# Kernel optimization log

Hardware: AMD Instinct MI355X
Metric: run time of the kernel (lower is better)

The kernel has to match this reference:

```python
import jax, jax.numpy as jnp
import numpy as np

NHEADS = 8
LN_EPS = 1e-5

def _layer_norm(x, g, b):
    mu = jnp.mean(x, axis=-1, keepdims=True)
    var = jnp.mean((x - mu) ** 2, axis=-1, keepdims=True)
    return (x - mu) * jax.lax.rsqrt(var + LN_EPS) * g + b

def setup_inputs() -> dict:
    key = jax.random.key(0)
    ks = jax.random.split(key, 12)
    B, L, D = 8, 1024, 512
    F = 2 * D  # ffn_dim = 2*dim
    std = 0.01  # init_weights: Linear weights ~ N(0, 0.01), biases zero
    inp = {
        'query': jax.random.normal(ks[0], (B, L, D), dtype=jnp.float32),
        'q_mask': jnp.ones((B, L), dtype=jnp.int32),
        'wq': jax.random.normal(ks[1], (D, D), dtype=jnp.float32) * std,
        'bq': jnp.zeros((D,), dtype=jnp.float32),
        'wk': jax.random.normal(ks[2], (D, D), dtype=jnp.float32) * std,
        'bk': jnp.zeros((D,), dtype=jnp.float32),
        'wv': jax.random.normal(ks[3], (D, D), dtype=jnp.float32) * std,
        'bv': jnp.zeros((D,), dtype=jnp.float32),
        'wo': jax.random.normal(ks[4], (D, D), dtype=jnp.float32) * std,
        'bo': jnp.zeros((D,), dtype=jnp.float32),
        'ln1_g': jnp.ones((D,), dtype=jnp.float32),
        'ln1_b': jnp.zeros((D,), dtype=jnp.float32),
        'w1': jax.random.normal(ks[5], (D, F), dtype=jnp.float32) * std,
        'b1': jnp.zeros((F,), dtype=jnp.float32),
        'w2': jax.random.normal(ks[6], (F, D), dtype=jnp.float32) * std,
        'b2': jnp.zeros((D,), dtype=jnp.float32),
        'ln2_g': jnp.ones((D,), dtype=jnp.float32),
        'ln2_b': jnp.zeros((D,), dtype=jnp.float32),
    }
    return inp

def reference(query, q_mask, wq, bq, wk, bk, wv, bv, wo, bo, ln1_g, ln1_b, w1, b1, w2, b2, ln2_g, ln2_b):
    B, L, D = query.shape
    H = NHEADS
    dh = D // H
    residual = query
    # projections (dropout in eval mode -> identity)
    q = query @ wq + bq
    k = query @ wk + bk
    v = query @ wv + bv
    # faithful to torch .view(batch*nheads, -1, dim_head) (no head transpose)
    q = q.reshape(B * H, L, dh)
    k = k.reshape(B * H, L, dh)
    v = v.reshape(B * H, L, dh)
    # faithful to torch mask.repeat(nheads, 1) -> tile along batch dim
    mf = q_mask.astype(jnp.float32)
    qm = jnp.tile(mf, (H, 1))  # [B*H, L]
    km = qm
    mask = qm[:, :, None] * km[:, None, :]  # [B*H, L, L] outer product
    scores = jnp.einsum('bqd,bkd->bqk', q, k) / np.sqrt(dh).astype(np.float32)
    A = jnp.where(mask == 0, 0.0, jnp.exp(scores))  # masked_fill(-inf).exp()
    A_sum = jnp.maximum(jnp.sum(A, axis=-1, keepdims=True), 1.0)
    attn = A / A_sum
    context = jnp.einsum('bqk,bkd->bqd', attn, v).reshape(B, L, H * dh)
    out = context @ wo + bo
    out = _layer_norm(residual + out, ln1_g, ln1_b)
    # positional-wise FFN: Linear -> ReLU -> Linear, residual + LayerNorm
    ffn = jax.nn.relu(out @ w1 + b1) @ w2 + b2
    out2 = _layer_norm(out + ffn, ln2_g, ln2_b)
    return (out2, q_mask, query, query, q_mask)
```

## Files before the change

kernel.cpp:

```cpp
#include <hip/hip_runtime.h>
#include <hip/hip_bf16.h>

typedef __hip_bfloat16 bf16;
typedef __attribute__((ext_vector_type(4))) float f32x4;
typedef __attribute__((ext_vector_type(8))) short s16x8;

#define MFMA(a, b, c) __builtin_amdgcn_mfma_f32_16x16x32_bf16((a), (b), (c), 0, 0, 0)

__device__ __forceinline__ void g2l16(const bf16* g, bf16* l) {
  __builtin_amdgcn_global_load_lds((const __attribute__((address_space(1))) void*)g,
                                   (__attribute__((address_space(3))) void*)l,
                                   16, 0, 0);
}
__device__ __forceinline__ bf16 cvt_bf(float f) { return __float2bfloat16(f); }
__device__ __forceinline__ float bf2f(bf16 h) { return __bfloat162float(h); }

__global__ __launch_bounds__(256)
void wcvt_all_k(const float* __restrict__ wq, const float* __restrict__ wk,
                const float* __restrict__ wv, const float* __restrict__ wo,
                const float* __restrict__ w1, const float* __restrict__ w2,
                bf16* __restrict__ wqkvT, bf16* __restrict__ woT,
                bf16* __restrict__ w1T, bf16* __restrict__ w2T)
{
  __shared__ float tl[32][33];
  const int bid = blockIdx.x;
  const float* W; bf16* Wt; int K, N, tile;
  if (bid < 768)        { int s = bid >> 8; W = s==0?wq:(s==1?wk:wv);
                          Wt = wqkvT + s*262144; K = 512; N = 512; tile = bid & 255; }
  else if (bid < 1024)  { W = wo; Wt = woT; K = 512;  N = 512;  tile = bid - 768; }
  else if (bid < 1536)  { W = w1; Wt = w1T; K = 512;  N = 1024; tile = bid - 1024; }
  else                  { W = w2; Wt = w2T; K = 1024; N = 512;  tile = bid - 1536; }
  const int nx = N >> 5;
  const int n0 = (tile % nx) * 32, k0 = (tile / nx) * 32;
  const int tx = threadIdx.x & 31, ty = threadIdx.x >> 5;
#pragma unroll
  for (int i = 0; i < 32; i += 8)
    tl[ty + i][tx] = W[(size_t)(k0 + ty + i) * N + n0 + tx];
  __syncthreads();
#pragma unroll
  for (int i = 0; i < 32; i += 8)
    Wt[(size_t)(n0 + ty + i) * K + k0 + tx] = cvt_bf(tl[tx][ty + i]);
}

__global__ __launch_bounds__(256)
void cvt_k(const float* __restrict__ in, bf16* __restrict__ o)
{
  const int i = (blockIdx.x * 256 + threadIdx.x) * 8;
  float4 a = *(const float4*)(in + i);
  float4 b = *(const float4*)(in + i + 4);
  union { bf16 h[8]; s16x8 v; } u;
  u.h[0] = cvt_bf(a.x); u.h[1] = cvt_bf(a.y); u.h[2] = cvt_bf(a.z); u.h[3] = cvt_bf(a.w);
  u.h[4] = cvt_bf(b.x); u.h[5] = cvt_bf(b.y); u.h[6] = cvt_bf(b.z); u.h[7] = cvt_bf(b.w);
  *(s16x8*)(o + i) = u.v;
}

template<int BN, int EPI>
__global__ __launch_bounds__(256, 2)
void gemm_k(const bf16* __restrict__ A, const bf16* __restrict__ Bt,
            const float* __restrict__ b0, const float* __restrict__ b1,
            const float* __restrict__ b2,
            const float* __restrict__ rF, const bf16* __restrict__ rB,
            bf16* __restrict__ C0, bf16* __restrict__ C1, bf16* __restrict__ C2,
            int M, int Nout, int K)
{
  constexpr int NI = BN / 32;
  __shared__ bf16 As[128 * 64];
  __shared__ bf16 Bs[BN * 64];
  const int tid = threadIdx.x;
  const int wave = tid >> 6, lane = tid & 63;
  const int g = lane >> 4, c = lane & 15;
  const int m0 = blockIdx.x * 128, n0 = blockIdx.y * BN;
  const int wm = (wave >> 1) * 64, wn = (wave & 1) * (BN / 2);
  const int srl = lane >> 3;
  const int csub = ((lane & 7) ^ (lane >> 3)) * 8;

  f32x4 acc[4][NI];
#pragma unroll
  for (int i = 0; i < 4; ++i)
#pragma unroll
    for (int j = 0; j < NI; ++j) acc[i][j] = (f32x4)0.f;

  for (int k0 = 0; k0 < K; k0 += 64) {
#pragma unroll
    for (int is = 0; is < 4; ++is) {
      const int tr = wave * 32 + is * 8;
      g2l16(A + (size_t)(m0 + tr + srl) * K + (k0 + csub), As + tr * 64);
    }
#pragma unroll
    for (int is = 0; is < BN / 32; ++is) {
      const int tr = wave * (BN / 4) + is * 8;
      g2l16(Bt + (size_t)(n0 + tr + srl) * K + (k0 + csub), Bs + tr * 64);
    }
    __syncthreads();
#pragma unroll
    for (int ks = 0; ks < 2; ++ks) {
      s16x8 af[4], bfr[NI];
#pragma unroll
      for (int i = 0; i < 4; ++i) {
        const int ar = wm + i * 16 + c;
        af[i] = *(const s16x8*)((const char*)As + ar * 128 + ((ks * 4 + g) ^ (ar & 7)) * 16);
      }
#pragma unroll
      for (int i = 0; i < NI; ++i) {
        const int br = wn + i * 16 + c;
        bfr[i] = *(const s16x8*)((const char*)Bs + br * 128 + ((ks * 4 + g) ^ (br & 7)) * 16);
      }
#pragma unroll
      for (int mi = 0; mi < 4; ++mi)
#pragma unroll
        for (int ni = 0; ni < NI; ++ni)
          acc[mi][ni] = MFMA(af[mi], bfr[ni], acc[mi][ni]);
    }
    __syncthreads();
  }

  bf16* Cp; const float* bp; int colbase;
  if constexpr (EPI == 0) {
    const int seg = n0 >> 9;
    Cp = seg == 0 ? C0 : (seg == 1 ? C1 : C2);
    bp = seg == 0 ? b0 : (seg == 1 ? b1 : b2);
    colbase = n0 & 511;
  } else { Cp = C0; bp = b0; colbase = n0; }

#pragma unroll
  for (int ni = 0; ni < NI; ++ni) {
    const int col = colbase + wn + ni * 16 + c;
    const float bv = bp[col];
#pragma unroll
    for (int mi = 0; mi < 4; ++mi) {
#pragma unroll
      for (int r = 0; r < 4; ++r) {
        const int row = m0 + wm + mi * 16 + g * 4 + r;
        float v = acc[mi][ni][r] + bv;
        if constexpr (EPI == 1) v += rF[(size_t)row * Nout + col];
        if constexpr (EPI == 2) v = fmaxf(v, 0.f);
        if constexpr (EPI == 3) v += bf2f(rB[(size_t)row * Nout + col]);
        Cp[(size_t)row * Nout + col] = cvt_bf(v);
      }
    }
  }
}

__global__ __launch_bounds__(256)
void vtr_k(const bf16* __restrict__ V, bf16* __restrict__ Vt)
{
  __shared__ bf16 tl[64][72];
  const int bh = blockIdx.y, kt = blockIdx.x;
  const int r = threadIdx.x >> 2, c = threadIdx.x & 3;
  const bf16* src = V + (size_t)bh * 65536 + (size_t)(kt * 64 + r) * 64 + c * 16;
  *(s16x8*)&tl[r][c * 16]     = *(const s16x8*)(src);
  *(s16x8*)&tl[r][c * 16 + 8] = *(const s16x8*)(src + 8);
  __syncthreads();
  union { bf16 h[8]; s16x8 v; } u0, u1;
#pragma unroll
  for (int j = 0; j < 8; ++j) { u0.h[j] = tl[c * 16 + j][r]; u1.h[j] = tl[c * 16 + 8 + j][r]; }
  bf16* dst = Vt + (size_t)bh * 65536 + (size_t)r * 1024 + kt * 64 + c * 16;
  *(s16x8*)dst = u0.v;
  *(s16x8*)(dst + 8) = u1.v;
}

__global__ __launch_bounds__(256, 2)
void attn_k(const bf16* __restrict__ Q, const bf16* __restrict__ Kp,
            const bf16* __restrict__ Vt, const int* __restrict__ mask,
            bf16* __restrict__ ctx)
{
  __shared__ bf16 Ks[2][64 * 64];
  __shared__ bf16 Vs[2][64 * 64];
  __shared__ __align__(16) float koff[1024];
  const int lane = threadIdx.x & 63, wave = threadIdx.x >> 6;
  const int g = lane >> 4, c = lane & 15;
  const int wg = blockIdx.x;
  const int swz = (wg & 7) * 64 + (wg >> 3);
  const int qb = swz & 7, bh = swz >> 3;
  const int q0w = qb * 128 + wave * 32;
  const bf16* Qg = Q  + (size_t)bh * 65536;
  const bf16* Kg = Kp + (size_t)bh * 65536;
  const bf16* Vg = Vt + (size_t)bh * 65536;
  const int* mrow = mask + (bh & 7) * 1024;

  {
    const int i = threadIdx.x * 4;
    int4 m4 = *(const int4*)(mrow + i);
    f32x4 kv;
    kv[0] = m4.x ? 0.f : -1e30f;
    kv[1] = m4.y ? 0.f : -1e30f;
    kv[2] = m4.z ? 0.f : -1e30f;
    kv[3] = m4.w ? 0.f : -1e30f;
    *(f32x4*)&koff[i] = kv;
  }

  s16x8 qa[2][2];
#pragma unroll
  for (int qs = 0; qs < 2; ++qs)
#pragma unroll
    for (int h = 0; h < 2; ++h)
      qa[qs][h] = *(const s16x8*)(Qg + (size_t)(q0w + qs * 16 + c) * 64 + h * 32 + g * 8);

  float qm[2][4];
#pragma unroll
  for (int qs = 0; qs < 2; ++qs)
#pragma unroll
    for (int r = 0; r < 4; ++r)
      qm[qs][r] = mrow[q0w + qs * 16 + g * 4 + r] ? 1.f : 0.f;

  s16x8 ones;
#pragma unroll
  for (int i = 0; i < 8; ++i) ones[i] = (short)0x3F80;

  f32x4 acc[2][4], asum[2];
#pragma unroll
  for (int qs = 0; qs < 2; ++qs) {
    asum[qs] = (f32x4)0.f;
#pragma unroll
    for (int db = 0; db < 4; ++db) acc[qs][db] = (f32x4)0.f;
  }

  const int rl = lane >> 3, ch = lane & 7;
  const int schunk = (ch ^ rl) * 8;

  auto STAGE = [&](int kt, int buf) {
#pragma unroll
    for (int rnd = 0; rnd < 2; ++rnd) {
      const int rb = wave * 16 + rnd * 8;
      const int l = rb + rl;
      const int i16 = l & 15, kbb = l >> 4;
      const int srow = ((kbb >> 1) << 5) + ((i16 >> 2) << 3) + ((kbb & 1) << 2) + (i16 & 3);
      g2l16(Kg + (size_t)(kt * 64 + srow) * 64 + schunk, &Ks[buf][rb * 64]);
      g2l16(Vg + (size_t)l * 1024 + kt * 64 + schunk, &Vs[buf][rb * 64]);
    }
  };

  STAGE(0, 0);
  __syncthreads();

  for (int kt = 0; kt < 16; ++kt) {
    const int cur = kt & 1;
    if (kt < 15) STAGE(kt + 1, cur ^ 1);

    union { unsigned w[8]; s16x8 v[2]; } pr[2];

#pragma unroll
    for (int kb = 0; kb < 4; ++kb) {
      const int krow = kb * 16 + c;
      const char* kbase = (const char*)&Ks[cur][0] + krow * 128;
      const s16x8 kf0 = *(const s16x8*)(kbase + ((g    ) ^ (c & 7)) * 16);
      const s16x8 kf1 = *(const s16x8*)(kbase + ((g + 4) ^ (c & 7)) * 16);
      const f32x4 ko = *(const f32x4*)&koff[kt * 64 + ((kb >> 1) << 5) + (g << 3) + ((kb & 1) << 2)];
#pragma unroll
      for (int qs = 0; qs < 2; ++qs) {
        f32x4 z = (f32x4)0.f;
        z = MFMA(kf0, qa[qs][0], z);
        z = MFMA(kf1, qa[qs][1], z);
        union { bf16 h[4]; unsigned u[2]; } eh;
#pragma unroll
        for (int r = 0; r < 4; ++r)
          eh.h[r] = cvt_bf(__expf(fmaf(z[r], 0.125f, ko[r])));
        pr[qs].w[kb * 2]     = eh.u[0];
        pr[qs].w[kb * 2 + 1] = eh.u[1];
      }
    }

#pragma unroll
    for (int kk = 0; kk < 2; ++kk) {
      s16x8 vf[4];
#pragma unroll
      for (int db = 0; db < 4; ++db)
        vf[db] = *(const s16x8*)((const char*)&Vs[cur][0] + (db * 16 + c) * 128 + ((4 * kk + g) ^ (c & 7)) * 16);
#pragma unroll
      for (int qs = 0; qs < 2; ++qs) {
        const s16x8 pa = pr[qs].v[kk];
        asum[qs] = MFMA(pa, ones, asum[qs]);
#pragma unroll
        for (int db = 0; db < 4; ++db)
          acc[qs][db] = MFMA(pa, vf[db], acc[qs][db]);
      }
    }
    __syncthreads();
  }

#pragma unroll
  for (int qs = 0; qs < 2; ++qs)
#pragma unroll
    for (int r = 0; r < 4; ++r) {
      const float inv = qm[qs][r] / fmaxf(asum[qs][r], 1.f);
      const size_t qr = q0w + qs * 16 + g * 4 + r;
#pragma unroll
      for (int db = 0; db < 4; ++db)
        ctx[(size_t)bh * 65536 + qr * 64 + db * 16 + c] = cvt_bf(acc[qs][db][r] * inv);
    }
}

template<int INB, int OUTF, int OUTB>
__global__ __launch_bounds__(256)
void ln_k(const void* __restrict__ xin, const float* __restrict__ g,
          const float* __restrict__ bb, float* __restrict__ of, bf16* __restrict__ ob)
{
  const int row = blockIdx.x * 4 + (threadIdx.x >> 6);
  const int lane = threadIdx.x & 63;
  float xv[8];
  if constexpr (INB) {
    union { s16x8 v; bf16 h[8]; } u;
    u.v = *(const s16x8*)((const bf16*)xin + (size_t)row * 512 + lane * 8);
#pragma unroll
    for (int j = 0; j < 8; ++j) xv[j] = bf2f(u.h[j]);
  } else {
    const float* xr = (const float*)xin + (size_t)row * 512 + lane * 8;
    float4 a = *(const float4*)xr, b = *(const float4*)(xr + 4);
    xv[0]=a.x; xv[1]=a.y; xv[2]=a.z; xv[3]=a.w; xv[4]=b.x; xv[5]=b.y; xv[6]=b.z; xv[7]=b.w;
  }
  float s = 0.f, q = 0.f;
#pragma unroll
  for (int j = 0; j < 8; ++j) { s += xv[j]; q += xv[j] * xv[j]; }
#pragma unroll
  for (int m = 1; m < 64; m <<= 1) { s += __shfl_xor(s, m); q += __shfl_xor(q, m); }
  const float mu = s * (1.f / 512.f);
  const float var = q * (1.f / 512.f) - mu * mu;
  const float rs = rsqrtf(var + 1e-5f);
  float4 g0 = *(const float4*)(g + lane * 8),  g1 = *(const float4*)(g + lane * 8 + 4);
  float4 b0 = *(const float4*)(bb + lane * 8), b1 = *(const float4*)(bb + lane * 8 + 4);
  float gv[8] = {g0.x, g0.y, g0.z, g0.w, g1.x, g1.y, g1.z, g1.w};
  float bv[8] = {b0.x, b0.y, b0.z, b0.w, b1.x, b1.y, b1.z, b1.w};
  float ov[8];
#pragma unroll
  for (int j = 0; j < 8; ++j) ov[j] = (xv[j] - mu) * rs * gv[j] + bv[j];
  if constexpr (OUTF) {
    float4 o0 = {ov[0], ov[1], ov[2], ov[3]};
    float4 o1 = {ov[4], ov[5], ov[6], ov[7]};
    float* outr = of + (size_t)row * 512 + lane * 8;
    *(float4*)outr = o0;
    *(float4*)(outr + 4) = o1;
  }
  if constexpr (OUTB) {
    union { bf16 h[8]; s16x8 v; } u;
#pragma unroll
    for (int j = 0; j < 8; ++j) u.h[j] = cvt_bf(ov[j]);
    *(s16x8*)(ob + (size_t)row * 512 + lane * 8) = u.v;
  }
}

__global__ __launch_bounds__(256)
void mask_k(const int* __restrict__ m, float* __restrict__ out)
{
  const int i = blockIdx.x * 256 + threadIdx.x;
  const float v = (float)m[i];
  out[4194304 + i] = v;
  out[12591104 + i] = v;
}

extern "C" void kernel_launch(void* const* d_in, const int* in_sizes, int n_in,
                              void* d_out, int out_size, void* d_ws, size_t ws_size,
                              hipStream_t stream)
{
  const float* query = (const float*)d_in[0];
  const int*   qmask = (const int*)d_in[1];
  const float* wq = (const float*)d_in[2];
  const float* bq = (const float*)d_in[3];
  const float* wk = (const float*)d_in[4];
  const float* bk = (const float*)d_in[5];
  const float* wv = (const float*)d_in[6];
  const float* bv = (const float*)d_in[7];
  const float* wo = (const float*)d_in[8];
  const float* bo = (const float*)d_in[9];
  const float* ln1g = (const float*)d_in[10];
  const float* ln1b = (const float*)d_in[11];
  const float* w1 = (const float*)d_in[12];
  const float* b1 = (const float*)d_in[13];
  const float* w2 = (const float*)d_in[14];
  const float* b2 = (const float*)d_in[15];
  const float* ln2g = (const float*)d_in[16];
  const float* ln2b = (const float*)d_in[17];
  float* out = (float*)d_out;
  char* ws = (char*)d_ws;
  char* ob = (char*)d_out;

  bf16* wqkvT = (bf16*)(ws);
  bf16* woT   = (bf16*)(ws + 1572864);
  bf16* w1T   = (bf16*)(ws + 2097152);
  bf16* w2T   = (bf16*)(ws + 3145728);

  char* R0 = ob;
  char* R1 = ob + 16809984;
  char* R2 = ob + 33587200;
  bf16*  qb    = (bf16*)R0;
  bf16*  ctx   = (bf16*)R0;
  bf16*  x1b   = (bf16*)R0;
  bf16*  Qb    = (bf16*)R1;
  bf16*  Kb    = (bf16*)(R1 + 8388608);
  bf16*  attnr = (bf16*)R1;
  bf16*  hbuf  = (bf16*)R1;
  bf16*  Vb    = (bf16*)R2;
  bf16*  VtG   = (bf16*)(R2 + 8388608);
  bf16*  ybuf  = (bf16*)R2;

  const dim3 blk(256);

  wcvt_all_k<<<2048, blk, 0, stream>>>(wq, wk, wv, wo, w1, w2, wqkvT, woT, w1T, w2T);
  cvt_k<<<2048, blk, 0, stream>>>(query, qb);

  gemm_k<128, 0><<<dim3(64, 12), blk, 0, stream>>>(qb, wqkvT, bq, bk, bv,
      nullptr, nullptr, Qb, Kb, Vb, 8192, 512, 512);

  vtr_k<<<dim3(16, 64), blk, 0, stream>>>(Vb, VtG);

  attn_k<<<512, blk, 0, stream>>>(Qb, Kb, VtG, qmask, ctx);

  gemm_k<64, 1><<<dim3(64, 8), blk, 0, stream>>>(ctx, woT, bo, nullptr, nullptr,
      query, nullptr, attnr, nullptr, nullptr, 8192, 512, 512);

  ln_k<1, 0, 1><<<2048, blk, 0, stream>>>(attnr, ln1g, ln1b, nullptr, x1b);

  gemm_k<128, 2><<<dim3(64, 8), blk, 0, stream>>>(x1b, w1T, b1, nullptr, nullptr,
      nullptr, nullptr, hbuf, nullptr, nullptr, 8192, 1024, 512);

  gemm_k<64, 3><<<dim3(64, 8), blk, 0, stream>>>(hbuf, w2T, b2, nullptr, nullptr,
      nullptr, x1b, ybuf, nullptr, nullptr, 8192, 512, 1024);

  ln_k<1, 1, 0><<<2048, blk, 0, stream>>>(ybuf, ln2g, ln2b, out, nullptr);

  mask_k<<<32, blk, 0, stream>>>(qmask, out);
  hipMemcpyAsync(out + 4202496, query, 16777216, hipMemcpyDeviceToDevice, stream);
  hipMemcpyAsync(out + 8396800, query, 16777216, hipMemcpyDeviceToDevice, stream);
}
```

Baseline: 225.6 us.

## Fuse query passthrough copies into prep kernel and add XCD-aware GEMM tile mapping

Adds a prep kernel that converts the query to bf16 and, in the same pass, writes the two fp32 passthrough copies of the query and both mask outputs. This removes two device memcpys and a separate mask kernel. When the workspace is large enough, intermediates move to the workspace so the passthrough outputs can be written early without being overwritten. GEMM launches become 1D with a block-index remap that gives each XCD a group of adjacent M tiles, aiming for better L2 locality. The fallback path keeps the old output-buffer aliasing.

```diff
diff --git a/kernel.cpp b/kernel.cpp
--- a/kernel.cpp
+++ b/kernel.cpp
@@ -43,6 +43,31 @@
 }
 
 __global__ __launch_bounds__(256)
+void prep_k(const float* __restrict__ query, const int* __restrict__ qmask,
+            bf16* __restrict__ qb, float* __restrict__ out)
+{
+  const int bid = blockIdx.x;
+  if (bid < 2048) {
+    const int i = bid * 2048 + threadIdx.x * 8;
+    float4 a = *(const float4*)(query + i);
+    float4 b = *(const float4*)(query + i + 4);
+    union { bf16 h[8]; s16x8 v; } u;
+    u.h[0] = cvt_bf(a.x); u.h[1] = cvt_bf(a.y); u.h[2] = cvt_bf(a.z); u.h[3] = cvt_bf(a.w);
+    u.h[4] = cvt_bf(b.x); u.h[5] = cvt_bf(b.y); u.h[6] = cvt_bf(b.z); u.h[7] = cvt_bf(b.w);
+    *(s16x8*)(qb + i) = u.v;
+    float* o1 = out + 4202496 + i;
+    float* o2 = out + 8396800 + i;
+    *(float4*)o1 = a; *(float4*)(o1 + 4) = b;
+    *(float4*)o2 = a; *(float4*)(o2 + 4) = b;
+  } else {
+    const int j = (bid - 2048) * 256 + threadIdx.x;
+    const float v = (float)qmask[j];
+    out[4194304 + j] = v;
+    out[12591104 + j] = v;
+  }
+}
+
+__global__ __launch_bounds__(256)
 void cvt_k(const float* __restrict__ in, bf16* __restrict__ o)
 {
   const int i = (blockIdx.x * 256 + threadIdx.x) * 8;
@@ -61,7 +86,7 @@
             const float* __restrict__ b2,
             const float* __restrict__ rF, const bf16* __restrict__ rB,
             bf16* __restrict__ C0, bf16* __restrict__ C1, bf16* __restrict__ C2,
-            int M, int Nout, int K)
+            int Nout, int K)
 {
   constexpr int NI = BN / 32;
   __shared__ bf16 As[128 * 64];
@@ -69,7 +94,10 @@
   const int tid = threadIdx.x;
   const int wave = tid >> 6, lane = tid & 63;
   const int g = lane >> 4, c = lane & 15;
-  const int m0 = blockIdx.x * 128, n0 = blockIdx.y * BN;
+  const int wgid = blockIdx.x;
+  const int xcd = wgid & 7, idx = wgid >> 3;
+  const int m0 = (xcd * 8 + (idx & 7)) * 128;
+  const int n0 = (idx >> 3) * BN;
   const int wm = (wave >> 1) * 64, wn = (wave & 1) * (BN / 2);
   const int srl = lane >> 3;
   const int csub = ((lane & 7) ^ (lane >> 3)) * 8;
@@ -371,53 +399,73 @@
   const float* ln2b = (const float*)d_in[17];
   float* out = (float*)d_out;
   char* ws = (char*)d_ws;
-  char* ob = (char*)d_out;
 
   bf16* wqkvT = (bf16*)(ws);
   bf16* woT   = (bf16*)(ws + 1572864);
   bf16* w1T   = (bf16*)(ws + 2097152);
   bf16* w2T   = (bf16*)(ws + 3145728);
 
-  char* R0 = ob;
-  char* R1 = ob + 16809984;
-  char* R2 = ob + 33587200;
-  bf16*  qb    = (bf16*)R0;
-  bf16*  ctx   = (bf16*)R0;
-  bf16*  x1b   = (bf16*)R0;
-  bf16*  Qb    = (bf16*)R1;
-  bf16*  Kb    = (bf16*)(R1 + 8388608);
-  bf16*  attnr = (bf16*)R1;
-  bf16*  hbuf  = (bf16*)R1;
-  bf16*  Vb    = (bf16*)R2;
-  bf16*  VtG   = (bf16*)(R2 + 8388608);
-  bf16*  ybuf  = (bf16*)R2;
-
   const dim3 blk(256);
 
-  wcvt_all_k<<<2048, blk, 0, stream>>>(wq, wk, wv, wo, w1, w2, wqkvT, woT, w1T, w2T);
-  cvt_k<<<2048, blk, 0, stream>>>(query, qb);
-
-  gemm_k<128, 0><<<dim3(64, 12), blk, 0, stream>>>(qb, wqkvT, bq, bk, bv,
-      nullptr, nullptr, Qb, Kb, Vb, 8192, 512, 512);
-
-  vtr_k<<<dim3(16, 64), blk, 0, stream>>>(Vb, VtG);
-
-  attn_k<<<512, blk, 0, stream>>>(Qb, Kb, VtG, qmask, ctx);
-
-  gemm_k<64, 1><<<dim3(64, 8), blk, 0, stream>>>(ctx, woT, bo, nullptr, nullptr,
-      query, nullptr, attnr, nullptr, nullptr, 8192, 512, 512);
-
-  ln_k<1, 0, 1><<<2048, blk, 0, stream>>>(attnr, ln1g, ln1b, nullptr, x1b);
-
-  gemm_k<128, 2><<<dim3(64, 8), blk, 0, stream>>>(x1b, w1T, b1, nullptr, nullptr,
-      nullptr, nullptr, hbuf, nullptr, nullptr, 8192, 1024, 512);
-
-  gemm_k<64, 3><<<dim3(64, 8), blk, 0, stream>>>(hbuf, w2T, b2, nullptr, nullptr,
-      nullptr, x1b, ybuf, nullptr, nullptr, 8192, 512, 1024);
-
-  ln_k<1, 1, 0><<<2048, blk, 0, stream>>>(ybuf, ln2g, ln2b, out, nullptr);
-
-  mask_k<<<32, blk, 0, stream>>>(qmask, out);
-  hipMemcpyAsync(out + 4202496, query, 16777216, hipMemcpyDeviceToDevice, stream);
-  hipMemcpyAsync(out + 8396800, query, 16777216, hipMemcpyDeviceToDevice, stream);
-}
+  if (ws_size >= (size_t)96468992) {
+    bf16*  qb    = (bf16*)(ws + 4194304);
+    bf16*  Qb    = (bf16*)(ws + 12582912);
+    bf16*  Kb    = (bf16*)(ws + 20971520);
+    bf16*  Vb    = (bf16*)(ws + 29360128);
+    bf16*  VtG   = (bf16*)(ws + 37748736);
+    bf16*  ctx   = (bf16*)(ws + 46137344);
+    bf16*  attnr = (bf16*)(ws + 54525952);
+    bf16*  x1b   = (bf16*)(ws + 62914560);
+    bf16*  hbuf  = (bf16*)(ws + 71303168);
+    bf16*  ybuf  = (bf16*)(ws + 88080384);
+
+    wcvt_all_k<<<2048, blk, 0, stream>>>(wq, wk, wv, wo, w1, w2, wqkvT, woT, w1T, w2T);
+    prep_k<<<2080, blk, 0, stream>>>(query, qmask, qb, out);
+
+    gemm_k<128, 0><<<768, blk, 0, stream>>>(qb, wqkvT, bq, bk, bv,
+        nullptr, nullptr, Qb, Kb, Vb, 512, 512);
+    vtr_k<<<dim3(16, 64), blk, 0, stream>>>(Vb, VtG);
+    attn_k<<<512, blk, 0, stream>>>(Qb, Kb, VtG, qmask, ctx);
+    gemm_k<64, 1><<<512, blk, 0, stream>>>(ctx, woT, bo, nullptr, nullptr,
+        query, nullptr, attnr, nullptr, nullptr, 512, 512);
+    ln_k<1, 0, 1><<<2048, blk, 0, stream>>>(attnr, ln1g, ln1b, nullptr, x1b);
+    gemm_k<128, 2><<<512, blk, 0, stream>>>(x1b, w1T, b1, nullptr, nullptr,
+        nullptr, nullptr, hbuf, nullptr, nullptr, 1024, 512);
+    gemm_k<64, 3><<<512, blk, 0, stream>>>(hbuf, w2T, b2, nullptr, nullptr,
+        nullptr, x1b, ybuf, nullptr, nullptr, 512, 1024);
+    ln_k<1, 1, 0><<<2048, blk, 0, stream>>>(ybuf, ln2g, ln2b, out, nullptr);
+  } else {
+    char* ob = (char*)d_out;
+    char* R0 = ob;
+    char* R1 = ob + 16809984;
+    char* R2 = ob + 33587200;
+    bf16*  qb    = (bf16*)R0;
+    bf16*  ctx   = (bf16*)R0;
+    bf16*  x1b   = (bf16*)R0;
+    bf16*  Qb    = (bf16*)R1;
+    bf16*  Kb    = (bf16*)(R1 + 8388608);
+    bf16*  attnr = (bf16*)R1;
+    bf16*  hbuf  = (bf16*)R1;
+    bf16*  Vb    = (bf16*)R2;
+    bf16*  VtG   = (bf16*)(R2 + 8388608);
+    bf16*  ybuf  = (bf16*)R2;
+
+    wcvt_all_k<<<2048, blk, 0, stream>>>(wq, wk, wv, wo, w1, w2, wqkvT, woT, w1T, w2T);
+    cvt_k<<<2048, blk, 0, stream>>>(query, qb);
+    gemm_k<128, 0><<<768, blk, 0, stream>>>(qb, wqkvT, bq, bk, bv,
+        nullptr, nullptr, Qb, Kb, Vb, 512, 512);
+    vtr_k<<<dim3(16, 64), blk, 0, stream>>>(Vb, VtG);
+    attn_k<<<512, blk, 0, stream>>>(Qb, Kb, VtG, qmask, ctx);
+    gemm_k<64, 1><<<512, blk, 0, stream>>>(ctx, woT, bo, nullptr, nullptr,
+        query, nullptr, attnr, nullptr, nullptr, 512, 512);
+    ln_k<1, 0, 1><<<2048, blk, 0, stream>>>(attnr, ln1g, ln1b, nullptr, x1b);
+    gemm_k<128, 2><<<512, blk, 0, stream>>>(x1b, w1T, b1, nullptr, nullptr,
+        nullptr, nullptr, hbuf, nullptr, nullptr, 1024, 512);
+    gemm_k<64, 3><<<512, blk, 0, stream>>>(hbuf, w2T, b2, nullptr, nullptr,
+        nullptr, x1b, ybuf, nullptr, nullptr, 512, 1024);
+    ln_k<1, 1, 0><<<2048, blk, 0, stream>>>(ybuf, ln2g, ln2b, out, nullptr);
+    mask_k<<<32, blk, 0, stream>>>(qmask, out);
+    hipMemcpyAsync(out + 4202496, query, 16777216, hipMemcpyDeviceToDevice, stream);
+    hipMemcpyAsync(out + 8396800, query, 16777216, hipMemcpyDeviceToDevice, stream);
+  }
+}
```

Result: faster. 219.4 us (-2.8%).
